# Performance work log

Hardware: AMD Instinct MI355X
Metric: run time of the kernel (lower is better)

## Reference

```python
import jax, jax.numpy as jnp
import numpy as np
import math

DIM = 1536
HEAD_DIM = 128
N_HEADS = DIM // HEAD_DIM
B, S = 2, 2048
F, H, W = 8, 16, 16  # F*H*W == S
MAX_POS = 1024
EPS = 1e-6


def _make_freqs():
    # complex rotary freqs per Wan convention, split [22,21,21] over head_dim/2=64
    c = HEAD_DIM // 2
    sizes = [c - 2 * (c // 3), c // 3, c // 3]
    theta = 10000.0
    parts = []
    for s in sizes:
        inv = 1.0 / theta ** (np.arange(s, dtype=np.float64) / s)
        ang = np.arange(MAX_POS, dtype=np.float64)[:, None] * inv[None, :]
        parts.append(np.stack([np.cos(ang), np.sin(ang)], axis=-1))
    return jnp.asarray(np.concatenate(parts, axis=1), dtype=jnp.float32)  # [MAX_POS, 64, 2]


def setup_inputs() -> dict:
    key = jax.random.key(0)
    ks = jax.random.split(key, 12)
    std = 1.0 / math.sqrt(DIM)
    inp = {
        "x": jax.random.normal(ks[0], (B, S, DIM), jnp.float32),
        "seq_lens": jnp.full((B,), S, jnp.int32),
        "grid_sizes": jnp.tile(jnp.array([[F, H, W]], jnp.int32), (B, 1)),
        "freqs": _make_freqs(),
        "Wq": jax.random.normal(ks[1], (DIM, DIM), jnp.float32) * std,
        "bq": jnp.zeros((DIM,), jnp.float32),
        "Wk": jax.random.normal(ks[2], (DIM, DIM), jnp.float32) * std,
        "bk": jnp.zeros((DIM,), jnp.float32),
        "Wv": jax.random.normal(ks[3], (DIM, DIM), jnp.float32) * std,
        "bv": jnp.zeros((DIM,), jnp.float32),
        "Wo": jax.random.normal(ks[4], (DIM, DIM), jnp.float32) * std,
        "bo": jnp.zeros((DIM,), jnp.float32),
        "wq_norm": jnp.ones((DIM,), jnp.float32),
        "wk_norm": jnp.ones((DIM,), jnp.float32),
    }
    return inp


def _rmsnorm(x, w):
    x32 = x.astype(jnp.float32)
    return x32 * jax.lax.rsqrt(jnp.mean(x32 * x32, axis=-1, keepdims=True) + EPS) * w


def _rope_apply(x, grid_sizes, freqs):
    # x: [B, S, N, D]; grid sizes uniform across batch -> vectorized (no per-sample loop)
    f, h, w = (int(v) for v in np.asarray(grid_sizes)[0])
    s_rot = f * h * w
    Bx, Sx, N, D = x.shape
    c = D // 2
    s0, s1 = c - 2 * (c // 3), c // 3
    cos, sin = freqs[..., 0], freqs[..., 1]

    def grid_cs(t):  # build [s_rot, c] table
        tf = jnp.broadcast_to(t[:f, None, None, :s0], (f, h, w, s0))
        th = jnp.broadcast_to(t[None, :h, None, s0:s0 + s1], (f, h, w, s1))
        tw = jnp.broadcast_to(t[None, None, :w, s0 + s1:s0 + 2 * s1], (f, h, w, s1))
        return jnp.concatenate([tf, th, tw], axis=-1).reshape(s_rot, 1, c)

    fc, fs = grid_cs(cos), grid_cs(sin)  # [s_rot, 1, c]
    xr = x[:, :s_rot].astype(jnp.float32).reshape(Bx, s_rot, N, c, 2)
    a, b = xr[..., 0], xr[..., 1]
    out = jnp.stack([a * fc - b * fs, a * fs + b * fc], axis=-1).reshape(Bx, s_rot, N, D)
    if s_rot < Sx:
        out = jnp.concatenate([out, x[:, s_rot:].astype(jnp.float32)], axis=1)
    return out


def reference(x, seq_lens, grid_sizes, freqs, Wq, bq, Wk, bk, Wv, bv, Wo, bo, wq_norm, wk_norm):
    Bx, Sx, dim = x.shape
    N, D = N_HEADS, HEAD_DIM
    q = _rmsnorm(x @ Wq.T + bq, wq_norm).reshape(Bx, Sx, N, D)
    k = _rmsnorm(x @ Wk.T + bk, wk_norm).reshape(Bx, Sx, N, D)
    v = (x @ Wv.T + bv).reshape(Bx, Sx, N, D)
    q = _rope_apply(q, grid_sizes, freqs)
    k = _rope_apply(k, grid_sizes, freqs)
    scores = jnp.einsum("bsnd,btnd->bnst", q, k) / math.sqrt(D)  # [B,N,S,S]
    kmask = jnp.arange(Sx)[None, :] < seq_lens[:, None]          # [B,S] over keys
    scores = jnp.where(kmask[:, None, None, :], scores, -1e30)
    attn = jax.nn.softmax(scores, axis=-1)
    out = jnp.einsum("bnst,btnd->bsnd", attn, v).reshape(Bx, Sx, dim)
    return out @ Wo.T + bo
```

## Files before the change

### kernel.cpp

```cpp
#include <hip/hip_runtime.h>

typedef __attribute__((ext_vector_type(8))) short bf16x8;
typedef __attribute__((ext_vector_type(8))) unsigned short ushort8;
typedef __attribute__((ext_vector_type(4))) float f32x4;
typedef __attribute__((ext_vector_type(16))) float f32x16;
typedef unsigned short u16;
typedef unsigned int u32;

__device__ inline float bf2f(u16 u) {
    unsigned int x = ((unsigned int)u) << 16;
    float f; __builtin_memcpy(&f, &x, 4); return f;
}
__device__ inline u16 f2bf(float f) {
    unsigned int x; __builtin_memcpy(&x, &f, 4);
    unsigned int r = (x + 0x7FFFu + ((x >> 16) & 1u)) >> 16;
    return (u16)r;
}
__device__ inline u32 cvtpk(float lo, float hi) {
    u32 r;
    asm("v_cvt_pk_bf16_f32 %0, %1, %2" : "=v"(r) : "v"(lo), "v"(hi));
    return r;
}
__device__ inline void store_out(u16* p, float v) { *p = f2bf(v); }
__device__ inline void store_out(float* p, float v) { *p = v; }

__global__ __launch_bounds__(256) void f32_to_bf16_kernel(const float* __restrict__ src,
                                                          u16* __restrict__ dst, int n8) {
    int i = blockIdx.x * 256 + threadIdx.x;
    if (i >= n8) return;
    float4 a = *(const float4*)(src + (size_t)i * 8);
    float4 b = *(const float4*)(src + (size_t)i * 8 + 4);
    ushort8 o;
    o[0] = f2bf(a.x); o[1] = f2bf(a.y); o[2] = f2bf(a.z); o[3] = f2bf(a.w);
    o[4] = f2bf(b.x); o[5] = f2bf(b.y); o[6] = f2bf(b.z); o[7] = f2bf(b.w);
    *(ushort8*)(dst + (size_t)i * 8) = o;
}

__global__ __launch_bounds__(256) void wconv_kernel(const float* __restrict__ Wq, const float* __restrict__ Wk,
                                                    const float* __restrict__ Wv, const float* __restrict__ Wo,
                                                    u16* __restrict__ wqkv, u16* __restrict__ wob) {
    int i = blockIdx.x * 256 + threadIdx.x;
    int seg = i / 294912, j = i - seg * 294912;
    const float* src = (seg == 0) ? Wq : (seg == 1) ? Wk : (seg == 2) ? Wv : Wo;
    u16* dst = (seg < 3) ? (wqkv + (size_t)seg * 2359296) : wob;
    float4 a = *(const float4*)(src + (size_t)j * 8);
    float4 b = *(const float4*)(src + (size_t)j * 8 + 4);
    ushort8 o;
    o[0] = f2bf(a.x); o[1] = f2bf(a.y); o[2] = f2bf(a.z); o[3] = f2bf(a.w);
    o[4] = f2bf(b.x); o[5] = f2bf(b.y); o[6] = f2bf(b.z); o[7] = f2bf(b.w);
    *(ushort8*)(dst + (size_t)j * 8) = o;
}

__global__ __launch_bounds__(256) void build_rope_kernel(const float* __restrict__ freqs,
                                                         float* __restrict__ rope) {
    int i = blockIdx.x * 256 + threadIdx.x;
    int s = i >> 6, j = i & 63;
    int fi = s >> 8, hi = (s >> 4) & 15, wi = s & 15;
    int pos = (j < 22) ? fi : ((j < 43) ? hi : wi);
    rope[s * 128 + j * 2]     = freqs[pos * 128 + j * 2];
    rope[s * 128 + j * 2 + 1] = freqs[pos * 128 + j * 2 + 1];
}

template <typename OutT>
__global__ __launch_bounds__(256) void gemm_bt(const u16* __restrict__ A, const u16* __restrict__ Bw,
                                               const float* __restrict__ bias, OutT* __restrict__ C,
                                               int M, int N, int K) {
    __shared__ __align__(16) u16 As[3][4096];
    __shared__ __align__(16) u16 Bs[3][4096];
    const int tid = threadIdx.x;
    const int w = tid >> 6, l = tid & 63;
    const int lg = l >> 4, li = l & 15;
    const int row0 = blockIdx.x * 128, col0 = blockIdx.y * 128;
    const int wr = (w >> 1) * 64, wc = (w & 1) * 64;
    const int nt = K >> 5;

    f32x4 acc[4][4] = {};

    auto STAGE = [&](int bi, int t) {
        int k0 = t << 5;
#pragma unroll
        for (int c = 0; c < 2; ++c) {
            int idx = c * 256 + tid;
            int r = idx >> 2, col8 = (idx & 3) * 8;
            __builtin_amdgcn_global_load_lds(
                (const __attribute__((address_space(1))) void*)(A + (size_t)(row0 + r) * K + k0 + col8),
                (__attribute__((address_space(3))) void*)((char*)&As[0][0] + bi * 8192 + c * 4096 + w * 1024), 16, 0, 0);
            __builtin_amdgcn_global_load_lds(
                (const __attribute__((address_space(1))) void*)(Bw + (size_t)(col0 + r) * K + k0 + col8),
                (__attribute__((address_space(3))) void*)((char*)&Bs[0][0] + bi * 8192 + c * 4096 + w * 1024), 16, 0, 0);
        }
    };

    STAGE(0, 0);
    STAGE(1, 1);
    for (int tb = 0; tb < nt; tb += 3) {
#pragma unroll
        for (int j = 0; j < 3; ++j) {
            const int t = tb + j;
            if (t + 2 < nt) {
                STAGE((j + 2) % 3, t + 2);
                asm volatile("s_waitcnt vmcnt(8)" ::: "memory");
            } else if (t + 1 < nt) {
                asm volatile("s_waitcnt vmcnt(4)" ::: "memory");
            } else {
                asm volatile("s_waitcnt vmcnt(0)" ::: "memory");
            }
            __builtin_amdgcn_s_barrier();
            __builtin_amdgcn_sched_barrier(0);
            const u16* as = &As[j][0];
            const u16* bs = &Bs[j][0];
            bf16x8 af[4], bfr[4];
#pragma unroll
            for (int m = 0; m < 4; ++m) af[m] = *(const bf16x8*)(as + (wr + m * 16 + li) * 32 + lg * 8);
#pragma unroll
            for (int n = 0; n < 4; ++n) bfr[n] = *(const bf16x8*)(bs + (wc + n * 16 + li) * 32 + lg * 8);
#pragma unroll
            for (int m = 0; m < 4; ++m)
#pragma unroll
                for (int n = 0; n < 4; ++n)
                    acc[m][n] = __builtin_amdgcn_mfma_f32_16x16x32_bf16(af[m], bfr[n], acc[m][n], 0, 0, 0);
            __builtin_amdgcn_sched_barrier(0);
            __builtin_amdgcn_s_barrier();
        }
    }

#pragma unroll
    for (int m = 0; m < 4; ++m) {
#pragma unroll
        for (int n = 0; n < 4; ++n) {
#pragma unroll
            for (int j = 0; j < 4; ++j) {
                int r = row0 + wr + m * 16 + lg * 4 + j;
                int cc = col0 + wc + n * 16 + li;
                float v = acc[m][n][j] + bias[cc];
                store_out(&C[(size_t)r * N + cc], v);
            }
        }
    }
}

__global__ __launch_bounds__(256) void rmsrope_kernel(const u16* __restrict__ qkv,
                                                      const float* __restrict__ wq_n,
                                                      const float* __restrict__ wk_n,
                                                      const float* __restrict__ rope,
                                                      u16* __restrict__ qh, u16* __restrict__ kh) {
    int row = blockIdx.x;
    int b = row >> 11, s = row & 2047;
    int t = threadIdx.x;
    const u16* pr = qkv + (size_t)row * 4608;
    int c0 = t * 6;

    float q[6], k[6];
#pragma unroll
    for (int i = 0; i < 3; ++i) {
        ushort2 uq = *(const ushort2*)(pr + c0 + 2 * i);
        ushort2 uk = *(const ushort2*)(pr + 1536 + c0 + 2 * i);
        q[2 * i] = bf2f(uq.x); q[2 * i + 1] = bf2f(uq.y);
        k[2 * i] = bf2f(uk.x); k[2 * i + 1] = bf2f(uk.y);
    }
    float sq = 0.f, sk = 0.f;
#pragma unroll
    for (int i = 0; i < 6; ++i) { sq += q[i] * q[i]; sk += k[i] * k[i]; }
#pragma unroll
    for (int off = 32; off >= 1; off >>= 1) {
        sq += __shfl_down(sq, off);
        sk += __shfl_down(sk, off);
    }
    __shared__ float red[8];
    int w = t >> 6, l = t & 63;
    if (l == 0) { red[w] = sq; red[w + 4] = sk; }
    __syncthreads();
    float rq = rsqrtf((red[0] + red[1] + red[2] + red[3]) * (1.0f / 1536.0f) + 1e-6f);
    float rk = rsqrtf((red[4] + red[5] + red[6] + red[7]) * (1.0f / 1536.0f) + 1e-6f);

#pragma unroll
    for (int i = 0; i < 3; ++i) {
        int c = c0 + 2 * i;
        int h = c >> 7, d = c & 127;
        float cs = rope[s * 128 + d];
        float sn = rope[s * 128 + d + 1];
        float qa = q[2 * i] * rq * wq_n[c], qb = q[2 * i + 1] * rq * wq_n[c + 1];
        float ka = k[2 * i] * rk * wk_n[c], kb = k[2 * i + 1] * rk * wk_n[c + 1];
        size_t o = ((size_t)(b * 12 + h) * 2048 + s) * 128 + d;
        ushort2 qo, ko;
        qo.x = f2bf(qa * cs - qb * sn); qo.y = f2bf(qa * sn + qb * cs);
        ko.x = f2bf(ka * cs - kb * sn); ko.y = f2bf(ka * sn + kb * cs);
        *(ushort2*)(qh + o) = qo;
        *(ushort2*)(kh + o) = ko;
    }
}

__global__ __launch_bounds__(256) void vtrans_kernel(const u16* __restrict__ qkv,
                                                     u16* __restrict__ vt) {
    const int s0 = blockIdx.x * 64;
    const int d0 = blockIdx.y * 64;
    const int bh = blockIdx.z;
    const int b = bh / 12, h = bh % 12;
    const int t = threadIdx.x;

    __shared__ __align__(16) u16 L[64 * 72];

#pragma unroll
    for (int j = 0; j < 2; ++j) {
        int idx = j * 256 + t;
        int s = idx >> 3, c8 = idx & 7;
        ushort8 v8 = *(const ushort8*)(qkv + (size_t)(b * 2048 + s0 + s) * 4608 + 3072 + h * 128 + d0 + c8 * 8);
        int pb = c8 ^ ((s >> 3) & 7);
        *(ushort8*)(L + s * 72 + pb * 8) = v8;
    }
    __syncthreads();
#pragma unroll
    for (int j = 0; j < 2; ++j) {
        int idx = j * 256 + t;
        int d = idx >> 3, s8 = idx & 7;
        ushort8 o;
#pragma unroll
        for (int i = 0; i < 8; ++i) {
            int ps = s8 * 8 + i;
            int v4 = ps & 15;
            int ls = (ps & ~15) | (v4 & 3) | ((v4 & 4) << 1) | ((v4 & 8) >> 1);
            o[i] = L[ls * 72 + ((((d >> 3) ^ (ls >> 3)) & 7) << 3) + (d & 7)];
        }
        *(ushort8*)(vt + (size_t)bh * 128 * 2048 + (size_t)(d0 + d) * 2048 + s0 + s8 * 8) = o;
    }
}

__global__ __launch_bounds__(256, 2) void attn_kernel(const u16* __restrict__ qh, const u16* __restrict__ kh,
                                                      const u16* __restrict__ vt, const int* __restrict__ seq_lens,
                                                      u16* __restrict__ aout) {
    const int qt = blockIdx.x;
    const int bh = blockIdx.y;
    const int b = bh / 12, h = bh % 12;
    const int tid = threadIdx.x;
    const int w = tid >> 6, l = tid & 63;
    const int q5 = l & 31;
    const int hi = l >> 5;
    const int seqlen = seq_lens[b];

    __shared__ __align__(16) char smem[65536];

    const size_t hbase = (size_t)bh * 2048 * 128;
    const u16* kb = kh + hbase;
    const u16* vtb = vt + hbase;

    const int qrow = qt * 128 + w * 32 + q5;
    bf16x8 qf[8];
    {
        const u16* qp = qh + hbase + (size_t)qrow * 128 + hi * 8;
#pragma unroll
        for (int kd = 0; kd < 8; ++kd) qf[kd] = *(const bf16x8*)(qp + kd * 16);
    }

    auto STAGE = [&](int bi, int kv0) {
#pragma unroll
        for (int i = 0; i < 4; ++i) {
            int p = i * 256 + tid;
            int kr = p >> 4, kc = p & 15;
            __builtin_amdgcn_global_load_lds(
                (const __attribute__((address_space(1))) void*)(kb + (size_t)(kv0 + kr) * 128 + ((kc ^ (kr & 15)) << 3)),
                (__attribute__((address_space(3))) void*)(smem + bi * 16384 + i * 4096 + w * 1024), 16, 0, 0);
            int vr = p >> 3, vc = p & 7;
            __builtin_amdgcn_global_load_lds(
                (const __attribute__((address_space(1))) void*)(vtb + (size_t)vr * 2048 + kv0 + ((vc ^ (vr & 7)) << 3)),
                (__attribute__((address_space(3))) void*)(smem + 32768 + bi * 16384 + i * 4096 + w * 1024), 16, 0, 0);
        }
    };

    f32x16 oacc[4] = {};
    float m_run = -3e38f, l_run = 0.f;
    const float c2 = 0.08838834764831845f * 1.44269504088896341f;

    STAGE(0, 0);
    for (int t = 0; t < 32; ++t) {
        const int cur = t & 1;
        const int kv0 = t * 64;
        if (t < 31) {
            STAGE(cur ^ 1, kv0 + 64);
            asm volatile("s_waitcnt vmcnt(8)" ::: "memory");
        } else {
            asm volatile("s_waitcnt vmcnt(0)" ::: "memory");
        }
        __builtin_amdgcn_s_barrier();
        __builtin_amdgcn_sched_barrier(0);

        const u16* Ks = (const u16*)(smem + cur * 16384);
        const u16* Vs = (const u16*)(smem + 32768 + cur * 16384);

        f32x16 sacc[2] = {};
        __builtin_amdgcn_s_setprio(1);
#pragma unroll
        for (int tt = 0; tt < 2; ++tt) {
            int row = tt * 32 + q5;
#pragma unroll
            for (int kd = 0; kd < 8; ++kd) {
                int bk = (2 * kd + hi) ^ (q5 & 15);
                bf16x8 kf = *(const bf16x8*)(Ks + row * 128 + bk * 8);
                sacc[tt] = __builtin_amdgcn_mfma_f32_32x32x16_bf16(kf, qf[kd], sacc[tt], 0, 0, 0);
            }
        }
        __builtin_amdgcn_s_setprio(0);

        if (kv0 + 64 > seqlen) {
#pragma unroll
            for (int tt = 0; tt < 2; ++tt)
#pragma unroll
                for (int m = 0; m < 4; ++m)
#pragma unroll
                    for (int r = 0; r < 4; ++r) {
                        int kv = kv0 + tt * 32 + m * 8 + hi * 4 + r;
                        if (kv >= seqlen) sacc[tt][m * 4 + r] = -1e30f;
                    }
        }

        float pmax = sacc[0][0];
#pragma unroll
        for (int tt = 0; tt < 2; ++tt)
#pragma unroll
            for (int r = 0; r < 16; ++r) pmax = fmaxf(pmax, sacc[tt][r]);
        pmax = fmaxf(pmax, __shfl_xor(pmax, 32));

        int defer = __all(pmax <= m_run + 62.7f);
        if (!defer) {
            float mnew = fmaxf(m_run, pmax);
            float alpha = __builtin_amdgcn_exp2f((m_run - mnew) * c2);
#pragma unroll
            for (int dt = 0; dt < 4; ++dt)
#pragma unroll
                for (int r = 0; r < 16; ++r) oacc[dt][r] *= alpha;
            l_run *= alpha;
            m_run = mnew;
        }

        float ls = 0.f;
        u32 Wp[2][4][2];
#pragma unroll
        for (int tt = 0; tt < 2; ++tt)
#pragma unroll
            for (int m = 0; m < 4; ++m) {
                float p0 = __builtin_amdgcn_exp2f((sacc[tt][4 * m + 0] - m_run) * c2);
                float p1 = __builtin_amdgcn_exp2f((sacc[tt][4 * m + 1] - m_run) * c2);
                float p2 = __builtin_amdgcn_exp2f((sacc[tt][4 * m + 2] - m_run) * c2);
                float p3 = __builtin_amdgcn_exp2f((sacc[tt][4 * m + 3] - m_run) * c2);
                ls += (p0 + p1) + (p2 + p3);
                Wp[tt][m][0] = cvtpk(p0, p1);
                Wp[tt][m][1] = cvtpk(p2, p3);
            }
        ls += __shfl_xor(ls, 32);
        l_run += ls;

        __builtin_amdgcn_s_setprio(1);
#pragma unroll
        for (int tt = 0; tt < 2; ++tt)
#pragma unroll
            for (int c = 0; c < 2; ++c) {
                union { u32 u[4]; bf16x8 v; } pu;
                pu.u[0] = Wp[tt][2 * c][0]; pu.u[1] = Wp[tt][2 * c][1];
                pu.u[2] = Wp[tt][2 * c + 1][0]; pu.u[3] = Wp[tt][2 * c + 1][1];
                int bk = 4 * tt + 2 * c + hi;
#pragma unroll
                for (int dt = 0; dt < 4; ++dt) {
                    int drow = dt * 32 + q5;
                    int pb = bk ^ (drow & 7);
                    bf16x8 vf = *(const bf16x8*)(Vs + drow * 64 + pb * 8);
                    oacc[dt] = __builtin_amdgcn_mfma_f32_32x32x16_bf16(vf, pu.v, oacc[dt], 0, 0, 0);
                }
            }
        __builtin_amdgcn_s_setprio(0);
        __builtin_amdgcn_sched_barrier(0);
        __builtin_amdgcn_s_barrier();
    }

    __syncthreads();
    u32* Lq = (u32*)smem + w * 2144;
    float inv_l = 1.0f / l_run;
#pragma unroll
    for (int dt = 0; dt < 4; ++dt)
#pragma unroll
        for (int m = 0; m < 4; ++m) {
            u32 w0 = cvtpk(oacc[dt][4 * m + 0] * inv_l, oacc[dt][4 * m + 1] * inv_l);
            u32 w1 = cvtpk(oacc[dt][4 * m + 2] * inv_l, oacc[dt][4 * m + 3] * inv_l);
            int widx = dt * 16 + 4 * m + 2 * hi;
            Lq[q5 * 67 + widx] = w0;
            Lq[q5 * 67 + widx + 1] = w1;
        }
    __builtin_amdgcn_s_waitcnt(0);
#pragma unroll
    for (int pp = 0; pp < 8; ++pp) {
        int qq = pp * 4 + (l >> 4);
        int cc = l & 15;
        union { u32 u[4]; ushort8 v; } ou;
        ou.u[0] = Lq[qq * 67 + cc * 4 + 0];
        ou.u[1] = Lq[qq * 67 + cc * 4 + 1];
        ou.u[2] = Lq[qq * 67 + cc * 4 + 2];
        ou.u[3] = Lq[qq * 67 + cc * 4 + 3];
        size_t off = ((size_t)(b * 2048 + qt * 128 + w * 32 + qq)) * 1536 + h * 128 + cc * 8;
        *(ushort8*)(aout + off) = ou.v;
    }
}

extern "C" void kernel_launch(void* const* d_in, const int* in_sizes, int n_in,
                              void* d_out, int out_size, void* d_ws, size_t ws_size,
                              hipStream_t stream) {
    const float* x    = (const float*)d_in[0];
    const int* seqlen = (const int*)d_in[1];
    const float* freqs = (const float*)d_in[3];
    const float* Wq = (const float*)d_in[4];  const float* bq = (const float*)d_in[5];
    const float* Wk = (const float*)d_in[6];  const float* bk = (const float*)d_in[7];
    const float* Wv = (const float*)d_in[8];  const float* bv = (const float*)d_in[9];
    const float* Wo = (const float*)d_in[10]; const float* bo = (const float*)d_in[11];
    const float* wqn = (const float*)d_in[12];
    const float* wkn = (const float*)d_in[13];
    float* out = (float*)d_out;

    char* ws = (char*)d_ws;
    u16*   xb   = (u16*)(ws);
    u16*   wqkv = (u16*)(ws + 12582912);
    u16*   wob  = (u16*)(ws + 26738688);
    float* bqkv = (float*)(ws + 31457280);
    float* rope = (float*)(ws + 31475712);
    u16*   qkv  = (u16*)(ws + 32524288);
    u16*   qhb  = (u16*)(ws + 70273024);
    u16*   khb  = (u16*)(ws + 82855936);
    u16*   vtb  = (u16*)(ws + 95438848);
    u16*   aob  = (u16*)(ws + 108021760);

    f32_to_bf16_kernel<<<3072, 256, 0, stream>>>(x, xb, 786432);
    wconv_kernel<<<4608, 256, 0, stream>>>(Wq, Wk, Wv, Wo, wqkv, wob);
    hipMemcpyAsync(bqkv,        bq, 1536 * 4, hipMemcpyDeviceToDevice, stream);
    hipMemcpyAsync(bqkv + 1536, bk, 1536 * 4, hipMemcpyDeviceToDevice, stream);
    hipMemcpyAsync(bqkv + 3072, bv, 1536 * 4, hipMemcpyDeviceToDevice, stream);
    build_rope_kernel<<<512, 256, 0, stream>>>(freqs, rope);

    gemm_bt<u16><<<dim3(32, 36), 256, 0, stream>>>(xb, wqkv, bqkv, qkv, 4096, 4608, 1536);
    rmsrope_kernel<<<4096, 256, 0, stream>>>(qkv, wqn, wkn, rope, qhb, khb);
    vtrans_kernel<<<dim3(32, 2, 24), 256, 0, stream>>>(qkv, vtb);
    attn_kernel<<<dim3(16, 24), 256, 0, stream>>>(qhb, khb, vtb, seqlen, aob);
    gemm_bt<float><<<dim3(32, 12), 256, 0, stream>>>(aob, wob, bo, out, 4096, 1536, 1536);
}
```

Baseline: 228.5 us.

## Add 256x256-tile 8-wave GEMM for QKV projection and swizzle LDS layout

Adds a new GEMM kernel with 256x256 output tiles, 512 threads, BK=64 split into two half-tiles with double buffering, interleaved staging and MFMA phases, setprio around MFMA bursts, and an XCD-aware block swizzle. It is used for the fused QKV projection in place of the 128x128 kernel. It also XOR-swizzles the LDS chunk layout in the existing gemm_bt to reduce bank conflicts. The larger tiles raise operand reuse per block, but the grid shrinks to 288 blocks, which risks uneven load across CUs, and the kernel needs 128KB of LDS.

```diff
diff --git a/kernel.cpp b/kernel.cpp
--- a/kernel.cpp
+++ b/kernel.cpp
@@ -62,6 +62,138 @@
 }
 
 template <typename OutT>
+__global__ __launch_bounds__(512) void gemm256(const u16* __restrict__ A, const u16* __restrict__ Bw,
+                                               const float* __restrict__ bias, OutT* __restrict__ C,
+                                               int M, int N, int K, int nby) {
+    __shared__ __align__(16) char smem[131072];
+    const int tid = threadIdx.x;
+    const int wid = tid >> 6, l = tid & 63;
+    const int wr = wid >> 2, wc = wid & 3;
+    const int lg = l >> 4, li = l & 15;
+    const int nwg = gridDim.x;
+    const int cpx = nwg >> 3;
+    int swz = (blockIdx.x & 7) * cpx + (blockIdx.x >> 3);
+    const int row0 = (swz / nby) * 256, col0 = (swz % nby) * 256;
+    const int NT = K >> 6;
+
+    f32x4 acc[8][4] = {};
+
+    auto STAGE_HT = [&](int mat, int t, int kk) {
+        const u16* src = mat ? Bw : A;
+        const int r0 = mat ? col0 : row0;
+        const int base = (mat ? 65536 : 0) + (t & 1) * 32768 + kk * 16384;
+#pragma unroll
+        for (int j = 0; j < 2; ++j) {
+            int bi = j * 512 + tid;
+            int r = bi >> 2;
+            int clog = (bi & 3) ^ (r & 3);
+            __builtin_amdgcn_global_load_lds(
+                (const __attribute__((address_space(1))) void*)(src + (size_t)(r0 + r) * K + t * 64 + kk * 32 + clog * 8),
+                (__attribute__((address_space(3))) void*)(smem + base + j * 8192 + wid * 1024), 16, 0, 0);
+        }
+    };
+    auto LDA = [&](bf16x8* af, int t, int kk, int mh) {
+        const u16* R = (const u16*)(smem + (t & 1) * 32768 + kk * 16384);
+#pragma unroll
+        for (int mm = 0; mm < 4; ++mm) {
+            int row = wr * 128 + (mh * 4 + mm) * 16 + li;
+            af[mm] = *(const bf16x8*)(R + row * 32 + ((lg ^ (li & 3)) * 8));
+        }
+    };
+    auto LDB = [&](bf16x8* bf, int t, int kk) {
+        const u16* R = (const u16*)(smem + 65536 + (t & 1) * 32768 + kk * 16384);
+#pragma unroll
+        for (int nn = 0; nn < 4; ++nn) {
+            int row = wc * 64 + nn * 16 + li;
+            bf[nn] = *(const bf16x8*)(R + row * 32 + ((lg ^ (li & 3)) * 8));
+        }
+    };
+
+    STAGE_HT(0, 0, 0); STAGE_HT(1, 0, 0); STAGE_HT(0, 0, 1); STAGE_HT(1, 0, 1);
+    STAGE_HT(0, 1, 0); STAGE_HT(1, 1, 0);
+    asm volatile("s_waitcnt vmcnt(4)" ::: "memory");
+    __builtin_amdgcn_s_barrier();
+    __builtin_amdgcn_sched_barrier(0);
+
+    bf16x8 af[4], bf[4];
+    for (int t = 0; t < NT; ++t) {
+        LDA(af, t, 0, 0); LDB(bf, t, 0);
+        if (t + 1 < NT) STAGE_HT(0, t + 1, 1);
+        __builtin_amdgcn_s_barrier();
+        asm volatile("s_waitcnt lgkmcnt(0)" ::: "memory");
+        __builtin_amdgcn_sched_barrier(0);
+        __builtin_amdgcn_s_setprio(1);
+#pragma unroll
+        for (int mm = 0; mm < 4; ++mm)
+#pragma unroll
+            for (int nn = 0; nn < 4; ++nn)
+                acc[mm][nn] = __builtin_amdgcn_mfma_f32_16x16x32_bf16(af[mm], bf[nn], acc[mm][nn], 0, 0, 0);
+        __builtin_amdgcn_s_setprio(0);
+        __builtin_amdgcn_sched_barrier(0);
+        __builtin_amdgcn_s_barrier();
+        LDA(af, t, 0, 1);
+        if (t + 1 < NT) STAGE_HT(1, t + 1, 1);
+        __builtin_amdgcn_s_barrier();
+        asm volatile("s_waitcnt lgkmcnt(0)" ::: "memory");
+        __builtin_amdgcn_sched_barrier(0);
+        __builtin_amdgcn_s_setprio(1);
+#pragma unroll
+        for (int mm = 0; mm < 4; ++mm)
+#pragma unroll
+            for (int nn = 0; nn < 4; ++nn)
+                acc[4 + mm][nn] = __builtin_amdgcn_mfma_f32_16x16x32_bf16(af[mm], bf[nn], acc[4 + mm][nn], 0, 0, 0);
+        __builtin_amdgcn_s_setprio(0);
+        __builtin_amdgcn_sched_barrier(0);
+        __builtin_amdgcn_s_barrier();
+        LDA(af, t, 1, 0); LDB(bf, t, 1);
+        if (t + 2 < NT) STAGE_HT(0, t + 2, 0);
+        __builtin_amdgcn_s_barrier();
+        asm volatile("s_waitcnt lgkmcnt(0)" ::: "memory");
+        __builtin_amdgcn_sched_barrier(0);
+        __builtin_amdgcn_s_setprio(1);
+#pragma unroll
+        for (int mm = 0; mm < 4; ++mm)
+#pragma unroll
+            for (int nn = 0; nn < 4; ++nn)
+                acc[mm][nn] = __builtin_amdgcn_mfma_f32_16x16x32_bf16(af[mm], bf[nn], acc[mm][nn], 0, 0, 0);
+        __builtin_amdgcn_s_setprio(0);
+        __builtin_amdgcn_sched_barrier(0);
+        __builtin_amdgcn_s_barrier();
+        LDA(af, t, 1, 1);
+        if (t + 2 < NT) STAGE_HT(1, t + 2, 0);
+        __builtin_amdgcn_s_barrier();
+        asm volatile("s_waitcnt lgkmcnt(0)" ::: "memory");
+        __builtin_amdgcn_sched_barrier(0);
+        __builtin_amdgcn_s_setprio(1);
+#pragma unroll
+        for (int mm = 0; mm < 4; ++mm)
+#pragma unroll
+            for (int nn = 0; nn < 4; ++nn)
+                acc[4 + mm][nn] = __builtin_amdgcn_mfma_f32_16x16x32_bf16(af[mm], bf[nn], acc[4 + mm][nn], 0, 0, 0);
+        __builtin_amdgcn_s_setprio(0);
+        __builtin_amdgcn_sched_barrier(0);
+        if (t + 2 < NT) { asm volatile("s_waitcnt vmcnt(4)" ::: "memory"); }
+        else            { asm volatile("s_waitcnt vmcnt(0)" ::: "memory"); }
+        __builtin_amdgcn_s_barrier();
+        __builtin_amdgcn_sched_barrier(0);
+    }
+
+#pragma unroll
+    for (int m = 0; m < 8; ++m) {
+#pragma unroll
+        for (int n = 0; n < 4; ++n) {
+#pragma unroll
+            for (int j = 0; j < 4; ++j) {
+                int r = row0 + wr * 128 + m * 16 + lg * 4 + j;
+                int cc = col0 + wc * 64 + n * 16 + li;
+                float v = acc[m][n][j] + bias[cc];
+                store_out(&C[(size_t)r * N + cc], v);
+            }
+        }
+    }
+}
+
+template <typename OutT>
 __global__ __launch_bounds__(256) void gemm_bt(const u16* __restrict__ A, const u16* __restrict__ Bw,
                                                const float* __restrict__ bias, OutT* __restrict__ C,
                                                int M, int N, int K) {
@@ -81,12 +213,13 @@
 #pragma unroll
         for (int c = 0; c < 2; ++c) {
             int idx = c * 256 + tid;
-            int r = idx >> 2, col8 = (idx & 3) * 8;
+            int r = idx >> 2;
+            int clog = (idx & 3) ^ (r & 3);
             __builtin_amdgcn_global_load_lds(
-                (const __attribute__((address_space(1))) void*)(A + (size_t)(row0 + r) * K + k0 + col8),
+                (const __attribute__((address_space(1))) void*)(A + (size_t)(row0 + r) * K + k0 + clog * 8),
                 (__attribute__((address_space(3))) void*)((char*)&As[0][0] + bi * 8192 + c * 4096 + w * 1024), 16, 0, 0);
             __builtin_amdgcn_global_load_lds(
-                (const __attribute__((address_space(1))) void*)(Bw + (size_t)(col0 + r) * K + k0 + col8),
+                (const __attribute__((address_space(1))) void*)(Bw + (size_t)(col0 + r) * K + k0 + clog * 8),
                 (__attribute__((address_space(3))) void*)((char*)&Bs[0][0] + bi * 8192 + c * 4096 + w * 1024), 16, 0, 0);
         }
     };
@@ -111,9 +244,9 @@
             const u16* bs = &Bs[j][0];
             bf16x8 af[4], bfr[4];
 #pragma unroll
-            for (int m = 0; m < 4; ++m) af[m] = *(const bf16x8*)(as + (wr + m * 16 + li) * 32 + lg * 8);
-#pragma unroll
-            for (int n = 0; n < 4; ++n) bfr[n] = *(const bf16x8*)(bs + (wc + n * 16 + li) * 32 + lg * 8);
+            for (int m = 0; m < 4; ++m) af[m] = *(const bf16x8*)(as + (wr + m * 16 + li) * 32 + ((lg ^ (li & 3)) * 8));
+#pragma unroll
+            for (int n = 0; n < 4; ++n) bfr[n] = *(const bf16x8*)(bs + (wc + n * 16 + li) * 32 + ((lg ^ (li & 3)) * 8));
 #pragma unroll
             for (int m = 0; m < 4; ++m)
 #pragma unroll
@@ -431,7 +564,7 @@
     hipMemcpyAsync(bqkv + 3072, bv, 1536 * 4, hipMemcpyDeviceToDevice, stream);
     build_rope_kernel<<<512, 256, 0, stream>>>(freqs, rope);
 
-    gemm_bt<u16><<<dim3(32, 36), 256, 0, stream>>>(xb, wqkv, bqkv, qkv, 4096, 4608, 1536);
+    gemm256<u16><<<288, 512, 0, stream>>>(xb, wqkv, bqkv, qkv, 4096, 4608, 1536, 18);
     rmsrope_kernel<<<4096, 256, 0, stream>>>(qkv, wqn, wkn, rope, qhb, khb);
     vtrans_kernel<<<dim3(32, 2, 24), 256, 0, stream>>>(qkv, vtb);
     attn_kernel<<<dim3(16, 24), 256, 0, stream>>>(qhb, khb, vtb, seqlen, aob);
```

New measurement: 246.7 us. 7.9% more time.
